# Performance work log

Measured on AMD Instinct MI355X. Metric: run time of the kernel, lower is better.

The kernel has to match this reference:

```python
import jax, jax.numpy as jnp
import numpy as np

B, H, S, D = 2, 16, 2048, 64

def setup_inputs() -> dict:
    key = jax.random.key(0)
    kq, kk, kv, km = jax.random.split(key, 4)
    q = jax.random.normal(kq, (B, H, S, D), dtype=jnp.float32)
    k = jax.random.normal(kk, (B, H, S, D), dtype=jnp.float32)
    v = jax.random.normal(kv, (B, H, S, D), dtype=jnp.float32)
    mask = jax.random.randint(km, (B, 1, S, S), 0, 2, dtype=jnp.int32)
    return {"q": q, "k": k, "v": v, "mask": mask}

def reference(q, k, v, mask):
    d_model = q.shape[-1]
    # scores: [B, H, S, S]
    score = jnp.einsum('bhqd,bhkd->bhqk', q, k) / jnp.sqrt(jnp.float32(d_model))
    score = jnp.where(mask == 0, jnp.float32(-1e9), score)
    attn = jax.nn.softmax(score, axis=-1)
    return jnp.einsum('bhqk,bhkd->bhqd', attn, v)
```

## Files before the change

### kernel.cpp

```cpp
#include <hip/hip_runtime.h>
#include <hip/hip_bf16.h>


#define B_ 2
#define H_ 16
#define S_ 2048
#define D_ 64
#define BQ 128
#define NW 8
#define BK 64
#define NT (S_ / BK)
#define PADW 72
#define TILEB (BK * D_ * 2)

typedef __attribute__((ext_vector_type(4))) float f32x4;
typedef __attribute__((ext_vector_type(8))) short bf16x8;
typedef __attribute__((ext_vector_type(4))) short bf16x4;

#define QSCALE 0.1803368801111137f
#define MASKNEG (-1.4426950408889634e9f)

static __device__ __forceinline__ short f2bf(float f) {
  __hip_bfloat16 h = __float2bfloat16(f);
  short s; __builtin_memcpy(&s, &h, sizeof(s)); return s;
}
static __device__ __forceinline__ float fexp2(float x) {
  return __builtin_amdgcn_exp2f(x);
}
static __device__ __forceinline__ unsigned cvt_pk_bf16(float a, float b) {
  unsigned r;
  asm("v_cvt_pk_bf16_f32 %0, %1, %2" : "=v"(r) : "v"(a), "v"(b));
  return r;
}
static __device__ __forceinline__ void gload_lds16(const void* g, void* l) {
  __builtin_amdgcn_global_load_lds(
      (__attribute__((address_space(1))) void*)g,
      (__attribute__((address_space(3))) void*)l, 16, 0, 0);
}

__global__ __launch_bounds__(256)
void pack_all(const float* __restrict__ kg, const float* __restrict__ vg,
              const int* __restrict__ mg,
              short* __restrict__ kw, short* __restrict__ vw,
              unsigned long long* __restrict__ mwp) {
  __shared__ float sv[BK][D_ + 1];
  const int bx  = blockIdx.x;
  const int tid = threadIdx.x;

  if (bx < 1024) {
    const int t  = bx & 31;
    const int bh = bx >> 5;
    const float* kt = kg + ((size_t)bh * S_ + t * BK) * D_;
    const float* vt = vg + ((size_t)bh * S_ + t * BK) * D_;
    short* ko = kw + ((size_t)bh * NT + t) * (BK * D_);
    short* vo = vw + ((size_t)bh * NT + t) * (BK * D_);

    const int row = tid >> 2;
    const int swz = (row & 7) << 4;

    #pragma unroll
    for (int c = 0; c < 2; ++c) {
      const int x = (tid & 3) * 32 + c * 16;
      const int dsrc = (x ^ swz) >> 1;
      const float4 u0 = *(const float4*)(kt + row * D_ + dsrc);
      const float4 u1 = *(const float4*)(kt + row * D_ + dsrc + 4);
      uint4 w;
      w.x = cvt_pk_bf16(u0.x, u0.y); w.y = cvt_pk_bf16(u0.z, u0.w);
      w.z = cvt_pk_bf16(u1.x, u1.y); w.w = cvt_pk_bf16(u1.z, u1.w);
      *(uint4*)(ko + row * D_ + (x >> 1)) = w;
    }

    #pragma unroll
    for (int i = 0; i < 4; ++i) {
      const int id = tid + 256 * i;
      const int r = id >> 4, c4 = (id & 15) * 4;
      const float4 u = *(const float4*)(vt + r * D_ + c4);
      sv[r][c4] = u.x; sv[r][c4+1] = u.y; sv[r][c4+2] = u.z; sv[r][c4+3] = u.w;
    }
    __syncthreads();
    #pragma unroll
    for (int c = 0; c < 2; ++c) {
      const int x = (tid & 3) * 32 + c * 16;
      const int ksrc = (x ^ swz) >> 1;
      uint4 w;
      w.x = cvt_pk_bf16(sv[ksrc+0][row], sv[ksrc+1][row]);
      w.y = cvt_pk_bf16(sv[ksrc+2][row], sv[ksrc+3][row]);
      w.z = cvt_pk_bf16(sv[ksrc+4][row], sv[ksrc+5][row]);
      w.w = cvt_pk_bf16(sv[ksrc+6][row], sv[ksrc+7][row]);
      *(uint4*)(vo + row * D_ + (x >> 1)) = w;
    }
  } else {
    const int r4   = bx - 1024;
    const int wv   = tid >> 6;
    const int lane = tid & 63;
    const int row  = r4 * 4 + wv;
    const int* mr = mg + (size_t)row * S_;
    unsigned long long* out = mwp + (size_t)row * NT;
    #pragma unroll
    for (int g = 0; g < 8; ++g) {
      const int4 v = *(const int4*)(mr + g * 256 + lane * 4);
      const unsigned long long b0 = __ballot(v.x != 0);
      const unsigned long long b1 = __ballot(v.y != 0);
      const unsigned long long b2 = __ballot(v.z != 0);
      const unsigned long long b3 = __ballot(v.w != 0);
      if (lane < 4) {
        const int tl = lane;
        const unsigned long long u =
            ((b0 >> (16 * tl)) & 0xFFFFULL)
          | (((b1 >> (16 * tl)) & 0xFFFFULL) << 16)
          | (((b2 >> (16 * tl)) & 0xFFFFULL) << 32)
          | (((b3 >> (16 * tl)) & 0xFFFFULL) << 48);
        out[g * 4 + tl] = u;
      }
    }
  }
}

__global__ __launch_bounds__(512, 4)
void attn_main(const float* __restrict__ qg, const short* __restrict__ kw,
               const short* __restrict__ vw,
               const unsigned long long* __restrict__ mw,
               float* __restrict__ outg) {
  __shared__ short sKV[2][2][BK * D_];
  __shared__ short sP[NW][16][64];

  const int tid  = threadIdx.x;
  const int lane = tid & 63;
  const int wv   = tid >> 6;
  const int l15  = lane & 15;
  const int quad = lane >> 4;

  const int f  = blockIdx.y * 16 + blockIdx.x;
  const int nf = (f & 7) * 64 + (f >> 3);
  const int bh = nf >> 4;
  const int b  = bh >> 4;
  const int q0 = (nf & 15) * BQ;
  const int qw = q0 + wv * 16 + l15;

  bf16x8 qf[2];
  {
    const float* qrow = qg + ((size_t)bh * S_ + qw) * D_;
    #pragma unroll
    for (int ks = 0; ks < 2; ++ks) {
      const float4 u0 = *(const float4*)(qrow + ks*32 + quad*8);
      const float4 u1 = *(const float4*)(qrow + ks*32 + quad*8 + 4);
      bf16x8 fq;
      fq[0]=f2bf(u0.x*QSCALE); fq[1]=f2bf(u0.y*QSCALE);
      fq[2]=f2bf(u0.z*QSCALE); fq[3]=f2bf(u0.w*QSCALE);
      fq[4]=f2bf(u1.x*QSCALE); fq[5]=f2bf(u1.y*QSCALE);
      fq[6]=f2bf(u1.z*QSCALE); fq[7]=f2bf(u1.w*QSCALE);
      qf[ks] = fq;
    }
  }

  f32x4 O[4];
  #pragma unroll
  for (int dt = 0; dt < 4; ++dt) O[dt] = (f32x4){0.f, 0.f, 0.f, 0.f};
  float l = 0.f;

  const char* kt = (const char*)(kw + (size_t)bh * NT * BK * D_);
  const char* vt = (const char*)(vw + (size_t)bh * NT * BK * D_);
  const unsigned long long* mb = mw + ((size_t)b * S_ + qw) * NT;
  const int so = tid * 16;

  const int swz = (l15 & 7) << 4;
  const int ro0 = l15*128 + (( 0 + quad*16) ^ swz);
  const int ro1 = l15*128 + ((64 + quad*16) ^ swz);
  char* const spw = (char*)sP + wv*2048;

  gload_lds16(kt + so, (char*)sKV + so);
  gload_lds16(vt + so, (char*)sKV + 8192 + so);
  kt += TILEB; vt += TILEB;
  int cur = 0;
  __syncthreads();

  for (int t = 0; t < NT; ++t) {
    const unsigned long long m64 = mb[t];
    if (t < NT - 1) {
      const int nb = (cur ^ 1) << 14;
      gload_lds16(kt + so, (char*)sKV + nb + so);
      gload_lds16(vt + so, (char*)sKV + nb + 8192 + so);
      kt += TILEB; vt += TILEB;
    }
    const char* kb = (const char*)sKV + (cur << 14);
    const char* vb = kb + 8192;

    f32x4 st[4];
    __builtin_amdgcn_s_setprio(1);
    #pragma unroll
    for (int mt = 0; mt < 4; ++mt) {
      f32x4 acc = (f32x4){0.f, 0.f, 0.f, 0.f};
      const bf16x8 kf0 = *(const bf16x8*)(kb + mt*2048 + ro0);
      const bf16x8 kf1 = *(const bf16x8*)(kb + mt*2048 + ro1);
      acc = __builtin_amdgcn_mfma_f32_16x16x32_bf16(kf0, qf[0], acc, 0, 0, 0);
      acc = __builtin_amdgcn_mfma_f32_16x16x32_bf16(kf1, qf[1], acc, 0, 0, 0);
      st[mt] = acc;
    }
    __builtin_amdgcn_s_setprio(0);

    const unsigned xlo = ((unsigned)m64) >> quad;
    const unsigned xhi = ((unsigned)(m64 >> 32)) >> quad;
    #pragma unroll
    for (int mt = 0; mt < 4; ++mt) {
      float p0 = fexp2(st[mt].x);
      float p1 = fexp2(st[mt].y);
      float p2 = fexp2(st[mt].z);
      float p3 = fexp2(st[mt].w);
      const int a0 = __builtin_amdgcn_sbfe((int)xlo, mt*4,      1);
      const int a1 = __builtin_amdgcn_sbfe((int)xlo, mt*4 + 16, 1);
      const int a2 = __builtin_amdgcn_sbfe((int)xhi, mt*4,      1);
      const int a3 = __builtin_amdgcn_sbfe((int)xhi, mt*4 + 16, 1);
      p0 = __uint_as_float(__float_as_uint(p0) & (unsigned)a0);
      p1 = __uint_as_float(__float_as_uint(p1) & (unsigned)a1);
      p2 = __uint_as_float(__float_as_uint(p2) & (unsigned)a2);
      p3 = __uint_as_float(__float_as_uint(p3) & (unsigned)a3);
      l += (p0 + p1) + (p2 + p3);
      uint2 uu;
      uu.x = cvt_pk_bf16(p0, p1);
      uu.y = cvt_pk_bf16(p2, p3);
      *(uint2*)(spw + l15*128 + ((mt*32 + quad*8) ^ swz)) = uu;
    }

    asm volatile("s_waitcnt lgkmcnt(0)" ::: "memory");

    const bf16x8 pf0 = *(const bf16x8*)(spw + l15*128 + (( 0 + quad*16) ^ swz));
    const bf16x8 pf1 = *(const bf16x8*)(spw + l15*128 + ((64 + quad*16) ^ swz));
    __builtin_amdgcn_s_setprio(1);
    #pragma unroll
    for (int dt = 0; dt < 4; ++dt) {
      const bf16x8 vf0 = *(const bf16x8*)(vb + dt*2048 + ro0);
      const bf16x8 vf1 = *(const bf16x8*)(vb + dt*2048 + ro1);
      O[dt] = __builtin_amdgcn_mfma_f32_16x16x32_bf16(pf0, vf0, O[dt], 0, 0, 0);
      O[dt] = __builtin_amdgcn_mfma_f32_16x16x32_bf16(pf1, vf1, O[dt], 0, 0, 0);
    }
    __builtin_amdgcn_s_setprio(0);

    __syncthreads();
    cur ^= 1;
  }

  l += __shfl_xor(l, 16);
  l += __shfl_xor(l, 32);
  float ir[4];
  #pragma unroll
  for (int r = 0; r < 4; ++r) ir[r] = 1.0f / __shfl(l, quad*4 + r);

  float* ob = outg + ((size_t)bh * S_ + q0 + wv*16) * D_;
  #pragma unroll
  for (int dt = 0; dt < 4; ++dt) {
    ob[(quad*4 + 0)*D_ + dt*16 + l15] = O[dt].x * ir[0];
    ob[(quad*4 + 1)*D_ + dt*16 + l15] = O[dt].y * ir[1];
    ob[(quad*4 + 2)*D_ + dt*16 + l15] = O[dt].z * ir[2];
    ob[(quad*4 + 3)*D_ + dt*16 + l15] = O[dt].w * ir[3];
  }
}

__global__ __launch_bounds__(256, 4)
void attn_fallback(const float* __restrict__ qg, const float* __restrict__ kg,
                   const float* __restrict__ vg, const int* __restrict__ maskg,
                   float* __restrict__ outg) {
  __shared__ short sK[BK][PADW];
  __shared__ short sVT[D_][PADW];
  __shared__ short sP[4][16][PADW];

  const int tid  = threadIdx.x;
  const int lane = tid & 63;
  const int wv   = tid >> 6;
  const int l15  = lane & 15;
  const int quad = lane >> 4;

  const int bh = blockIdx.y;
  const int b  = bh >> 4;
  const int q0 = blockIdx.x * 64;
  const int qw = q0 + wv * 16 + l15;

  bf16x8 qf[2];
  {
    const float* qrow = qg + ((size_t)bh * S_ + qw) * D_;
    #pragma unroll
    for (int ks = 0; ks < 2; ++ks) {
      const float4 u0 = *(const float4*)(qrow + ks*32 + quad*8);
      const float4 u1 = *(const float4*)(qrow + ks*32 + quad*8 + 4);
      bf16x8 fq;
      fq[0]=f2bf(u0.x*QSCALE); fq[1]=f2bf(u0.y*QSCALE);
      fq[2]=f2bf(u0.z*QSCALE); fq[3]=f2bf(u0.w*QSCALE);
      fq[4]=f2bf(u1.x*QSCALE); fq[5]=f2bf(u1.y*QSCALE);
      fq[6]=f2bf(u1.z*QSCALE); fq[7]=f2bf(u1.w*QSCALE);
      qf[ks] = fq;
    }
  }

  f32x4 O[4];
  #pragma unroll
  for (int dt = 0; dt < 4; ++dt) O[dt] = (f32x4){0.f, 0.f, 0.f, 0.f};
  float m = -3.0e38f, l = 0.f;

  const float* kbase = kg + (size_t)bh * S_ * D_;
  const float* vbase = vg + (size_t)bh * S_ * D_;
  const int*   mrow  = maskg + ((size_t)b * S_ + qw) * S_;

  for (int t0 = 0; t0 < S_; t0 += BK) {
    __syncthreads();
    #pragma unroll
    for (int i = 0; i < 4; ++i) {
      const int id = tid + 256*i;
      const int key = id >> 4, d4 = (id & 15) * 4;
      const float4 u = *(const float4*)(kbase + (size_t)(t0 + key)*D_ + d4);
      bf16x4 w; w[0]=f2bf(u.x); w[1]=f2bf(u.y); w[2]=f2bf(u.z); w[3]=f2bf(u.w);
      *(bf16x4*)&sK[key][d4] = w;
    }
    #pragma unroll
    for (int i = 0; i < 2; ++i) {
      const int id = tid + 256*i;
      const int kp = id & 31, d4 = (id >> 5) * 4;
      const float4 a = *(const float4*)(vbase + (size_t)(t0 + 2*kp    )*D_ + d4);
      const float4 c = *(const float4*)(vbase + (size_t)(t0 + 2*kp + 1)*D_ + d4);
      const float av[4] = {a.x, a.y, a.z, a.w};
      const float cv[4] = {c.x, c.y, c.z, c.w};
      #pragma unroll
      for (int j = 0; j < 4; ++j) {
        const unsigned pk = (unsigned)(unsigned short)f2bf(av[j])
                          | ((unsigned)(unsigned short)f2bf(cv[j]) << 16);
        *(unsigned*)&sVT[d4 + j][2*kp] = pk;
      }
    }
    __syncthreads();

    int4 mk[4];
    #pragma unroll
    for (int mt = 0; mt < 4; ++mt)
      mk[mt] = *(const int4*)(mrow + t0 + mt*16 + quad*4);

    f32x4 st[4];
    #pragma unroll
    for (int mt = 0; mt < 4; ++mt) {
      f32x4 acc = (f32x4){0.f, 0.f, 0.f, 0.f};
      #pragma unroll
      for (int ks = 0; ks < 2; ++ks) {
        const bf16x8 kf = *(const bf16x8*)&sK[mt*16 + l15][ks*32 + quad*8];
        acc = __builtin_amdgcn_mfma_f32_16x16x32_bf16(kf, qf[ks], acc, 0, 0, 0);
      }
      st[mt] = acc;
    }

    float cmax = -3.0e38f;
    #pragma unroll
    for (int mt = 0; mt < 4; ++mt) {
      f32x4 s = st[mt];
      s.x = mk[mt].x ? s.x : MASKNEG;
      s.y = mk[mt].y ? s.y : MASKNEG;
      s.z = mk[mt].z ? s.z : MASKNEG;
      s.w = mk[mt].w ? s.w : MASKNEG;
      st[mt] = s;
      cmax = fmaxf(cmax, fmaxf(fmaxf(s.x, s.y), fmaxf(s.z, s.w)));
    }
    cmax = fmaxf(cmax, __shfl_xor(cmax, 16));
    cmax = fmaxf(cmax, __shfl_xor(cmax, 32));
    const float mnew  = fmaxf(m, cmax);
    const float alpha = fexp2(m - mnew);
    m = mnew;

    float lsum = 0.f;
    #pragma unroll
    for (int mt = 0; mt < 4; ++mt) {
      const float p0 = fexp2(st[mt].x - mnew);
      const float p1 = fexp2(st[mt].y - mnew);
      const float p2 = fexp2(st[mt].z - mnew);
      const float p3 = fexp2(st[mt].w - mnew);
      lsum += (p0 + p1) + (p2 + p3);
      bf16x4 pw; pw[0]=f2bf(p0); pw[1]=f2bf(p1); pw[2]=f2bf(p2); pw[3]=f2bf(p3);
      *(bf16x4*)&sP[wv][l15][mt*16 + quad*4] = pw;
    }
    lsum += __shfl_xor(lsum, 16);
    lsum += __shfl_xor(lsum, 32);
    l = l * alpha + lsum;

    const float ar0 = __shfl(alpha, quad*4 + 0);
    const float ar1 = __shfl(alpha, quad*4 + 1);
    const float ar2 = __shfl(alpha, quad*4 + 2);
    const float ar3 = __shfl(alpha, quad*4 + 3);
    #pragma unroll
    for (int dt = 0; dt < 4; ++dt) {
      O[dt].x *= ar0; O[dt].y *= ar1; O[dt].z *= ar2; O[dt].w *= ar3;
    }

    asm volatile("s_waitcnt lgkmcnt(0)" ::: "memory");

    const bf16x8 pf0 = *(const bf16x8*)&sP[wv][l15][quad*8];
    const bf16x8 pf1 = *(const bf16x8*)&sP[wv][l15][32 + quad*8];
    #pragma unroll
    for (int dt = 0; dt < 4; ++dt) {
      const bf16x8 vf0 = *(const bf16x8*)&sVT[dt*16 + l15][quad*8];
      const bf16x8 vf1 = *(const bf16x8*)&sVT[dt*16 + l15][32 + quad*8];
      O[dt] = __builtin_amdgcn_mfma_f32_16x16x32_bf16(pf0, vf0, O[dt], 0, 0, 0);
      O[dt] = __builtin_amdgcn_mfma_f32_16x16x32_bf16(pf1, vf1, O[dt], 0, 0, 0);
    }
  }

  float ir[4];
  #pragma unroll
  for (int r = 0; r < 4; ++r) ir[r] = 1.0f / __shfl(l, quad*4 + r);

  float* ob = outg + ((size_t)bh * S_ + q0 + wv*16) * D_;
  #pragma unroll
  for (int dt = 0; dt < 4; ++dt) {
    ob[(quad*4 + 0)*D_ + dt*16 + l15] = O[dt].x * ir[0];
    ob[(quad*4 + 1)*D_ + dt*16 + l15] = O[dt].y * ir[1];
    ob[(quad*4 + 2)*D_ + dt*16 + l15] = O[dt].z * ir[2];
    ob[(quad*4 + 3)*D_ + dt*16 + l15] = O[dt].w * ir[3];
  }
}

extern "C" void kernel_launch(void* const* d_in, const int* in_sizes, int n_in,
                              void* d_out, int out_size, void* d_ws, size_t ws_size,
                              hipStream_t stream) {
  const float* q    = (const float*)d_in[0];
  const float* k    = (const float*)d_in[1];
  const float* v    = (const float*)d_in[2];
  const int*   mask = (const int*)d_in[3];
  float* out = (float*)d_out;

  const size_t kvbytes = (size_t)B_ * H_ * S_ * D_ * 2;
  const size_t mbytes  = (size_t)B_ * S_ * NT * 8;
  const size_t need    = 2 * kvbytes + mbytes;

  if (d_ws != nullptr && ws_size >= need) {
    short* kwp = (short*)d_ws;
    short* vwp = (short*)((char*)d_ws + kvbytes);
    unsigned long long* mwp = (unsigned long long*)((char*)d_ws + 2 * kvbytes);
    pack_all<<<dim3(2048), 256, 0, stream>>>(k, v, mask, kwp, vwp, mwp);
    attn_main<<<dim3(S_ / BQ, B_ * H_), 512, 0, stream>>>(q, kwp, vwp, mwp, out);
  } else {
    attn_fallback<<<dim3(S_ / 64, B_ * H_), 256, 0, stream>>>(q, k, v, mask, out);
  }
}
```

Before: 165.8 us.

## Transpose P in registers via permlane swaps and compute row sums with MFMA

Drops the per-wave LDS staging buffer for the probability tile. The S-to-P layout transpose is now done in registers with v_permlane32/16_swap, which removes LDS writes, reads and a waitcnt from every key tile. The softmax denominator now comes from an extra MFMA against a ones vector, replacing the scalar adds and the final shuffles. That sum uses the bf16-rounded probabilities, so numerics shift slightly. Launch bounds now request 8 blocks per CU, which tightens register limits.

```diff
diff --git a/kernel.cpp b/kernel.cpp
--- a/kernel.cpp
+++ b/kernel.cpp
@@ -7,7 +7,6 @@
 #define S_ 2048
 #define D_ 64
 #define BQ 128
-#define NW 8
 #define BK 64
 #define NT (S_ / BK)
 #define PADW 72
@@ -16,6 +15,7 @@
 typedef __attribute__((ext_vector_type(4))) float f32x4;
 typedef __attribute__((ext_vector_type(8))) short bf16x8;
 typedef __attribute__((ext_vector_type(4))) short bf16x4;
+typedef __attribute__((ext_vector_type(4))) unsigned u32x4;
 
 #define QSCALE 0.1803368801111137f
 #define MASKNEG (-1.4426950408889634e9f)
@@ -36,6 +36,12 @@
   __builtin_amdgcn_global_load_lds(
       (__attribute__((address_space(1))) void*)g,
       (__attribute__((address_space(3))) void*)l, 16, 0, 0);
+}
+static __device__ __forceinline__ void perm32sw(unsigned& a, unsigned& b) {
+  asm("v_permlane32_swap_b32 %0, %1" : "+v"(a), "+v"(b));
+}
+static __device__ __forceinline__ void perm16sw(unsigned& a, unsigned& b) {
+  asm("v_permlane16_swap_b32 %0, %1" : "+v"(a), "+v"(b));
 }
 
 __global__ __launch_bounds__(256)
@@ -116,13 +122,12 @@
   }
 }
 
-__global__ __launch_bounds__(512, 4)
+__global__ __launch_bounds__(512, 8)
 void attn_main(const float* __restrict__ qg, const short* __restrict__ kw,
                const short* __restrict__ vw,
                const unsigned long long* __restrict__ mw,
                float* __restrict__ outg) {
   __shared__ short sKV[2][2][BK * D_];
-  __shared__ short sP[NW][16][64];
 
   const int tid  = threadIdx.x;
   const int lane = tid & 63;
@@ -153,10 +158,14 @@
     }
   }
 
+  bf16x8 onesf;
+  #pragma unroll
+  for (int j = 0; j < 8; ++j) onesf[j] = (short)0x3F80;
+
   f32x4 O[4];
   #pragma unroll
   for (int dt = 0; dt < 4; ++dt) O[dt] = (f32x4){0.f, 0.f, 0.f, 0.f};
-  float l = 0.f;
+  f32x4 Ol = (f32x4){0.f, 0.f, 0.f, 0.f};
 
   const char* kt = (const char*)(kw + (size_t)bh * NT * BK * D_);
   const char* vt = (const char*)(vw + (size_t)bh * NT * BK * D_);
@@ -166,7 +175,6 @@
   const int swz = (l15 & 7) << 4;
   const int ro0 = l15*128 + (( 0 + quad*16) ^ swz);
   const int ro1 = l15*128 + ((64 + quad*16) ^ swz);
-  char* const spw = (char*)sP + wv*2048;
 
   gload_lds16(kt + so, (char*)sKV + so);
   gload_lds16(vt + so, (char*)sKV + 8192 + so);
@@ -200,6 +208,7 @@
 
     const unsigned xlo = ((unsigned)m64) >> quad;
     const unsigned xhi = ((unsigned)(m64 >> 32)) >> quad;
+    uint2 U[4];
     #pragma unroll
     for (int mt = 0; mt < 4; ++mt) {
       float p0 = fexp2(st[mt].x);
@@ -214,17 +223,26 @@
       p1 = __uint_as_float(__float_as_uint(p1) & (unsigned)a1);
       p2 = __uint_as_float(__float_as_uint(p2) & (unsigned)a2);
       p3 = __uint_as_float(__float_as_uint(p3) & (unsigned)a3);
-      l += (p0 + p1) + (p2 + p3);
-      uint2 uu;
-      uu.x = cvt_pk_bf16(p0, p1);
-      uu.y = cvt_pk_bf16(p2, p3);
-      *(uint2*)(spw + l15*128 + ((mt*32 + quad*8) ^ swz)) = uu;
-    }
-
-    asm volatile("s_waitcnt lgkmcnt(0)" ::: "memory");
-
-    const bf16x8 pf0 = *(const bf16x8*)(spw + l15*128 + (( 0 + quad*16) ^ swz));
-    const bf16x8 pf1 = *(const bf16x8*)(spw + l15*128 + ((64 + quad*16) ^ swz));
+      U[mt].x = cvt_pk_bf16(p0, p1);
+      U[mt].y = cvt_pk_bf16(p2, p3);
+    }
+
+    unsigned w00 = U[0].x, w02 = U[1].x;
+    perm32sw(w00, w02); perm16sw(w00, w02);
+    unsigned w01 = U[0].y, w03 = U[1].y;
+    perm32sw(w01, w03); perm16sw(w01, w03);
+    unsigned w10 = U[2].x, w12 = U[3].x;
+    perm32sw(w10, w12); perm16sw(w10, w12);
+    unsigned w11 = U[2].y, w13 = U[3].y;
+    perm32sw(w11, w13); perm16sw(w11, w13);
+    bf16x8 pf0, pf1;
+    {
+      u32x4 t0 = (u32x4){w00, w01, w02, w03};
+      u32x4 t1 = (u32x4){w10, w11, w12, w13};
+      __builtin_memcpy(&pf0, &t0, 16);
+      __builtin_memcpy(&pf1, &t1, 16);
+    }
+
     __builtin_amdgcn_s_setprio(1);
     #pragma unroll
     for (int dt = 0; dt < 4; ++dt) {
@@ -233,17 +251,17 @@
       O[dt] = __builtin_amdgcn_mfma_f32_16x16x32_bf16(pf0, vf0, O[dt], 0, 0, 0);
       O[dt] = __builtin_amdgcn_mfma_f32_16x16x32_bf16(pf1, vf1, O[dt], 0, 0, 0);
     }
+    Ol = __builtin_amdgcn_mfma_f32_16x16x32_bf16(pf0, onesf, Ol, 0, 0, 0);
+    Ol = __builtin_amdgcn_mfma_f32_16x16x32_bf16(pf1, onesf, Ol, 0, 0, 0);
     __builtin_amdgcn_s_setprio(0);
 
     __syncthreads();
     cur ^= 1;
   }
 
-  l += __shfl_xor(l, 16);
-  l += __shfl_xor(l, 32);
   float ir[4];
-  #pragma unroll
-  for (int r = 0; r < 4; ++r) ir[r] = 1.0f / __shfl(l, quad*4 + r);
+  ir[0] = 1.0f / Ol.x; ir[1] = 1.0f / Ol.y;
+  ir[2] = 1.0f / Ol.z; ir[3] = 1.0f / Ol.w;
 
   float* ob = outg + ((size_t)bh * S_ + q0 + wv*16) * D_;
   #pragma unroll
```

Result: slower. 169.5 us (+2.2%).
